# Optimization experiments

Hardware: AMD Instinct MI355X
Metric: run time of the kernel (lower is better)

The kernel has to match this reference:

```python
import jax, jax.numpy as jnp
import numpy as np

MESSAGE_PASSES = 3
HID = 100        # hidden_node_features == message_size
EDGE_F = 4       # n_edge_features
OUT = 100        # readout output dim


def setup_inputs() -> dict:
    key = jax.random.key(0)
    ks = jax.random.split(key, 8)
    B, N = 32, 128
    nodes = jax.random.normal(ks[0], (B, N, HID), dtype=jnp.float32)
    edges = jax.random.uniform(ks[1], (B, N, N, EDGE_F), dtype=jnp.float32)
    s = 1.0 / np.sqrt(HID)
    Wv = jax.random.normal(ks[2], (HID, HID), dtype=jnp.float32) * s
    Ww = jax.random.normal(ks[3], (HID, HID), dtype=jnp.float32) * s
    We = jax.random.normal(ks[4], (EDGE_F, HID), dtype=jnp.float32) * (1.0 / np.sqrt(EDGE_F))
    Wu = jax.random.normal(ks[5], (2 * HID, HID), dtype=jnp.float32) * (1.0 / np.sqrt(2 * HID))
    Wr = jax.random.normal(ks[6], (2 * HID, OUT), dtype=jnp.float32) * (1.0 / np.sqrt(2 * HID))
    return {"nodes": nodes, "edges": edges, "Wv": Wv, "Ww": Ww, "We": We, "Wu": Wu, "Wr": Wr}


def reference(nodes, edges, Wv, Ww, We, Wu, Wr):
    # adjacency[b,v,w] = sum_e edges[b,v,w,e]; nonzero entries define the edge set
    adjacency = edges.sum(axis=-1)                       # [B,N,N]
    edge_mask = adjacency != 0                           # [B,N,N]
    node_mask = adjacency.sum(axis=-1) != 0              # [B,N]

    # edge feature projection is constant across message passes
    e_proj = jnp.einsum('bvwe,eh->bvwh', edges, We)      # [B,N,N,H]

    hidden = nodes                                       # hidden_node_features == node feat dim
    for _ in range(MESSAGE_PASSES):
        # message_terms for every (b, v, w) edge: relu(h_v Wv + h_w Ww + e_vw We)
        pre = (hidden @ Wv)[:, :, None, :] + (hidden @ Ww)[:, None, :, :] + e_proj
        mterms = jnp.where(edge_mask[..., None], jax.nn.relu(pre), 0.0)
        # (same_batch * same_node) matmul == segment-sum over neighbors w
        messages = mterms.sum(axis=2)                    # [B,N,H]
        # update only nodes that appear in the edge set (degree > 0)
        upd = jnp.tanh(jnp.concatenate([hidden, messages], axis=-1) @ Wu)
        hidden = jnp.where(node_mask[..., None], upd, hidden)

    # readout: masked sum-pool of per-node graph terms
    graph_terms = jax.nn.relu(jnp.concatenate([hidden, nodes], axis=-1) @ Wr)  # [B,N,OUT]
    output = jnp.where(node_mask[..., None], graph_terms, 0.0).sum(axis=1)     # [B,OUT]
    return output
```

## Files before the change

### kernel.cpp

```cpp
#include <hip/hip_runtime.h>
#include <math.h>

#define BATCH 32
#define N 128
#define H 100
#define EF 4

__global__ __launch_bounds__(128) void k_hw(const float* __restrict__ hidden,
                                            const float* __restrict__ Ww,
                                            float* __restrict__ hw) {
    const int row = blockIdx.x;
    const int t = threadIdx.x;
    __shared__ float hid[H];
    if (t < H) hid[t] = hidden[row * H + t];
    __syncthreads();
    if (t < H) {
        float acc = 0.f;
#pragma unroll 4
        for (int k = 0; k < H; ++k) acc = fmaf(hid[k], Ww[k * H + t], acc);
        hw[row * H + t] = acc;
    }
}

__global__ __launch_bounds__(128) void k_msg_upd(const float* __restrict__ edges,
                                                 const float* __restrict__ Wv,
                                                 const float* __restrict__ We,
                                                 const float* __restrict__ Wu,
                                                 const float* __restrict__ hw,
                                                 float* __restrict__ hidden,
                                                 float* __restrict__ node_mask) {
    const int row = blockIdx.x;
    const int b = row >> 7;
    const int t = threadIdx.x;

    __shared__ float hid[H];
    __shared__ float4 erow[N];
    __shared__ float asum[N];
    __shared__ float msg[H];
    __shared__ float nodesum;

    if (t < H) hid[t] = hidden[row * H + t];
    {
        const float4* e4 = (const float4*)(edges + (size_t)row * N * EF);
        float4 e = e4[t];
        erow[t] = e;
        asum[t] = ((e.x + e.y) + e.z) + e.w;
    }
    __syncthreads();

    if (t == 0) {
        float s = 0.f;
        for (int w = 0; w < N; ++w) s += asum[w];
        nodesum = s;
        node_mask[row] = (s != 0.f) ? 1.f : 0.f;
    }

    if (t < H) {
        float hv = 0.f;
#pragma unroll 4
        for (int k = 0; k < H; ++k) hv = fmaf(hid[k], Wv[k * H + t], hv);

        const float we0 = We[t];
        const float we1 = We[H + t];
        const float we2 = We[2 * H + t];
        const float we3 = We[3 * H + t];

        const float* hwb = hw + (size_t)b * N * H + t;
        float acc = 0.f;
#pragma unroll 4
        for (int w = 0; w < N; ++w) {
            const float4 e = erow[w];
            float pre = hv + hwb[w * H];
            pre = fmaf(e.x, we0, pre);
            pre = fmaf(e.y, we1, pre);
            pre = fmaf(e.z, we2, pre);
            pre = fmaf(e.w, we3, pre);
            acc += (asum[w] != 0.f) ? fmaxf(pre, 0.f) : 0.f;
        }
        msg[t] = acc;
    }
    __syncthreads();

    if (t < H) {
        float u = 0.f;
#pragma unroll 4
        for (int k = 0; k < H; ++k) u = fmaf(hid[k], Wu[k * H + t], u);
#pragma unroll 4
        for (int k = 0; k < H; ++k) u = fmaf(msg[k], Wu[(H + k) * H + t], u);
        const float newh = (nodesum != 0.f) ? tanhf(u) : hid[t];
        hidden[row * H + t] = newh;
    }
}

__global__ __launch_bounds__(128) void k_readout(const float* __restrict__ hidden,
                                                 const float* __restrict__ nodes,
                                                 const float* __restrict__ Wr,
                                                 const float* __restrict__ node_mask,
                                                 float* __restrict__ out) {
    const int row = blockIdx.x;
    const int b = row >> 7;
    const int t = threadIdx.x;
    __shared__ float hid[H];
    __shared__ float nod[H];
    if (t < H) {
        hid[t] = hidden[row * H + t];
        nod[t] = nodes[row * H + t];
    }
    __syncthreads();
    if (node_mask[row] == 0.f) return;
    if (t < H) {
        float u = 0.f;
#pragma unroll 4
        for (int k = 0; k < H; ++k) u = fmaf(hid[k], Wr[k * H + t], u);
#pragma unroll 4
        for (int k = 0; k < H; ++k) u = fmaf(nod[k], Wr[(H + k) * H + t], u);
        u = fmaxf(u, 0.f);
        atomicAdd(&out[b * H + t], u);
    }
}

extern "C" void kernel_launch(void* const* d_in, const int* in_sizes, int n_in,
                              void* d_out, int out_size, void* d_ws, size_t ws_size,
                              hipStream_t stream) {
    const float* nodes = (const float*)d_in[0];
    const float* edges = (const float*)d_in[1];
    const float* Wv    = (const float*)d_in[2];
    const float* Ww    = (const float*)d_in[3];
    const float* We    = (const float*)d_in[4];
    const float* Wu    = (const float*)d_in[5];
    const float* Wr    = (const float*)d_in[6];
    float* out = (float*)d_out;

    const int rows = BATCH * N;
    float* hidden = (float*)d_ws;
    float* hwbuf  = hidden + (size_t)rows * H;
    float* nmask  = hwbuf + (size_t)rows * H;

    hipMemcpyAsync(hidden, nodes, (size_t)rows * H * sizeof(float),
                   hipMemcpyDeviceToDevice, stream);
    hipMemsetAsync(d_out, 0, (size_t)out_size * sizeof(float), stream);

    for (int p = 0; p < 3; ++p) {
        k_hw<<<rows, 128, 0, stream>>>(hidden, Ww, hwbuf);
        k_msg_upd<<<rows, 128, 0, stream>>>(edges, Wv, We, Wu, hwbuf, hidden, nmask);
    }
    k_readout<<<rows, 128, 0, stream>>>(hidden, nodes, Wr, nmask, out);
}
```

Before: 238.1 us.

## Tile eight nodes per block, stage neighbor projections in LDS, fuse next-pass projection

Each block now processes eight nodes of one graph, with two output columns per thread. Neighbor hW rows are staged in shared memory in two 64-row halves and reused across the eight nodes, instead of every node re-reading all of hW from global memory. The next pass's hv/hw projections are fused into the update kernel using ping-pong hw buffers, and the node mask moves to a separate wave-reduction kernel. Readout reduces over the eight nodes in shared memory before issuing atomics. The cost is more shared memory per block (about 34 KB), some idle threads (448 threads for 400 active), and more workspace buffers.

```diff
diff --git a/kernel.cpp b/kernel.cpp
--- a/kernel.cpp
+++ b/kernel.cpp
@@ -1,121 +1,228 @@
 #include <hip/hip_runtime.h>
 #include <math.h>
 
-#define BATCH 32
-#define N 128
-#define H 100
-#define EF 4
-
-__global__ __launch_bounds__(128) void k_hw(const float* __restrict__ hidden,
-                                            const float* __restrict__ Ww,
-                                            float* __restrict__ hw) {
-    const int row = blockIdx.x;
-    const int t = threadIdx.x;
-    __shared__ float hid[H];
-    if (t < H) hid[t] = hidden[row * H + t];
-    __syncthreads();
-    if (t < H) {
-        float acc = 0.f;
-#pragma unroll 4
-        for (int k = 0; k < H; ++k) acc = fmaf(hid[k], Ww[k * H + t], acc);
-        hw[row * H + t] = acc;
-    }
-}
-
-__global__ __launch_bounds__(128) void k_msg_upd(const float* __restrict__ edges,
-                                                 const float* __restrict__ Wv,
-                                                 const float* __restrict__ We,
-                                                 const float* __restrict__ Wu,
-                                                 const float* __restrict__ hw,
-                                                 float* __restrict__ hidden,
-                                                 float* __restrict__ node_mask) {
-    const int row = blockIdx.x;
-    const int b = row >> 7;
-    const int t = threadIdx.x;
-
-    __shared__ float hid[H];
-    __shared__ float4 erow[N];
-    __shared__ float asum[N];
-    __shared__ float msg[H];
-    __shared__ float nodesum;
-
-    if (t < H) hid[t] = hidden[row * H + t];
-    {
-        const float4* e4 = (const float4*)(edges + (size_t)row * N * EF);
-        float4 e = e4[t];
-        erow[t] = e;
-        asum[t] = ((e.x + e.y) + e.z) + e.w;
-    }
-    __syncthreads();
-
-    if (t == 0) {
-        float s = 0.f;
-        for (int w = 0; w < N; ++w) s += asum[w];
-        nodesum = s;
-        node_mask[row] = (s != 0.f) ? 1.f : 0.f;
-    }
-
-    if (t < H) {
-        float hv = 0.f;
-#pragma unroll 4
-        for (int k = 0; k < H; ++k) hv = fmaf(hid[k], Wv[k * H + t], hv);
-
-        const float we0 = We[t];
-        const float we1 = We[H + t];
-        const float we2 = We[2 * H + t];
-        const float we3 = We[3 * H + t];
-
-        const float* hwb = hw + (size_t)b * N * H + t;
-        float acc = 0.f;
-#pragma unroll 4
-        for (int w = 0; w < N; ++w) {
-            const float4 e = erow[w];
-            float pre = hv + hwb[w * H];
-            pre = fmaf(e.x, we0, pre);
-            pre = fmaf(e.y, we1, pre);
-            pre = fmaf(e.z, we2, pre);
-            pre = fmaf(e.w, we3, pre);
-            acc += (asum[w] != 0.f) ? fmaxf(pre, 0.f) : 0.f;
-        }
-        msg[t] = acc;
-    }
-    __syncthreads();
-
-    if (t < H) {
-        float u = 0.f;
-#pragma unroll 4
-        for (int k = 0; k < H; ++k) u = fmaf(hid[k], Wu[k * H + t], u);
-#pragma unroll 4
-        for (int k = 0; k < H; ++k) u = fmaf(msg[k], Wu[(H + k) * H + t], u);
-        const float newh = (nodesum != 0.f) ? tanhf(u) : hid[t];
-        hidden[row * H + t] = newh;
-    }
-}
-
-__global__ __launch_bounds__(128) void k_readout(const float* __restrict__ hidden,
+#define B_   32
+#define N_   128
+#define H_   100
+#define VT   8
+#define TPB  448
+#define ROWS (B_ * N_)
+
+__global__ __launch_bounds__(256) void k_mask(const float* __restrict__ edges,
+                                              float* __restrict__ nmask) {
+    const int t = threadIdx.x, lane = t & 63, wv = t >> 6;
+    const int row = blockIdx.x * 4 + wv;
+    const float4* eg = (const float4*)(edges + (size_t)row * N_ * 4);
+    float4 e0 = eg[lane], e1 = eg[lane + 64];
+    float s = ((e0.x + e0.y) + (e0.z + e0.w)) + ((e1.x + e1.y) + (e1.z + e1.w));
+#pragma unroll
+    for (int off = 32; off > 0; off >>= 1) s += __shfl_down(s, off);
+    if (lane == 0) nmask[row] = (s != 0.f) ? 1.f : 0.f;
+}
+
+__global__ __launch_bounds__(TPB) void k_proj0(const float* __restrict__ nodes,
+                                               const float* __restrict__ Wv,
+                                               const float* __restrict__ Ww,
+                                               float* __restrict__ hv_out,
+                                               float* __restrict__ hw_out) {
+    __shared__ float hid_s[VT * H_];
+    const int b = blockIdx.y, v0 = blockIdx.x * VT;
+    const int t = threadIdx.x, v = t / 50, hp = t % 50;
+    const bool act = (v < VT);
+    const int row = b * N_ + v0 + (act ? v : 0);
+
+    const float4* ng = (const float4*)(nodes + (size_t)(b * N_ + v0) * H_);
+    for (int idx = t; idx < VT * 25; idx += TPB) ((float4*)hid_s)[idx] = ng[idx];
+    __syncthreads();
+    if (!act) return;
+
+    const float2* Wv2 = (const float2*)Wv;
+    const float2* Ww2 = (const float2*)Ww;
+    float va0 = 0, va1 = 0, wa0 = 0, wa1 = 0;
+    const float* hr = hid_s + v * H_;
+#pragma unroll 4
+    for (int k = 0; k < H_; ++k) {
+        const float hk = hr[k];
+        const float2 wv = Wv2[k * 50 + hp];
+        const float2 ww = Ww2[k * 50 + hp];
+        va0 = fmaf(hk, wv.x, va0); va1 = fmaf(hk, wv.y, va1);
+        wa0 = fmaf(hk, ww.x, wa0); wa1 = fmaf(hk, ww.y, wa1);
+    }
+    *(float2*)(hv_out + (size_t)row * H_ + hp * 2) = make_float2(va0, va1);
+    *(float2*)(hw_out + (size_t)row * H_ + hp * 2) = make_float2(wa0, wa1);
+}
+
+__global__ __launch_bounds__(TPB) void k_pass(const float* __restrict__ edges,
+                                              const float* __restrict__ Wv,
+                                              const float* __restrict__ Ww,
+                                              const float* __restrict__ We,
+                                              const float* __restrict__ Wu,
+                                              const float* hv_io,
+                                              const float* __restrict__ hw_in,
+                                              float* __restrict__ hw_out,
+                                              float* __restrict__ hidden,
+                                              const float* __restrict__ nmask,
+                                              int do_proj) {
+    __shared__ float  hw_s[64 * H_];
+    __shared__ float4 e_s[VT * 64];
+    __shared__ float  mask_s[VT * 64];
+    __shared__ float  hid_s[VT * H_];
+
+    const int b = blockIdx.y, v0 = blockIdx.x * VT;
+    const int t = threadIdx.x, v = t / 50, hp = t % 50;
+    const bool act = (v < VT);
+    const int row = b * N_ + v0 + (act ? v : 0);
+
+    float2 hv2 = make_float2(0.f, 0.f), we0, we1, we2, we3;
+    if (act) {
+        hv2 = *(const float2*)(hv_io + (size_t)row * H_ + hp * 2);
+        we0 = *(const float2*)(We + 0 * H_ + hp * 2);
+        we1 = *(const float2*)(We + 1 * H_ + hp * 2);
+        we2 = *(const float2*)(We + 2 * H_ + hp * 2);
+        we3 = *(const float2*)(We + 3 * H_ + hp * 2);
+    }
+    float a0 = 0.f, a1 = 0.f;
+
+    for (int half = 0; half < 2; ++half) {
+        const int w0 = half * 64;
+        __syncthreads();
+        {
+            const float4* hwg = (const float4*)(hw_in + (size_t)(b * N_ + w0) * H_);
+            float4* hws4 = (float4*)hw_s;
+            for (int idx = t; idx < 64 * 25; idx += TPB) hws4[idx] = hwg[idx];
+        }
+        {
+            const float4* eg = (const float4*)edges;
+            for (int idx = t; idx < VT * 64; idx += TPB) {
+                const int vv = idx >> 6, w = idx & 63;
+                const float4 e = eg[(size_t)(b * N_ + v0 + vv) * N_ + w0 + w];
+                e_s[vv * 64 + w] = e;
+                const float s = ((e.x + e.y) + (e.z + e.w));
+                mask_s[vv * 64 + w] = (s != 0.f) ? 1.f : 0.f;
+            }
+        }
+        if (half == 0) {
+            const float4* hg = (const float4*)(hidden + (size_t)(b * N_ + v0) * H_);
+            for (int idx = t; idx < VT * 25; idx += TPB) ((float4*)hid_s)[idx] = hg[idx];
+        }
+        __syncthreads();
+        if (act) {
+            const float4* ev = e_s + v * 64;
+            const float*  mv = mask_s + v * 64;
+#pragma unroll 4
+            for (int w = 0; w < 64; ++w) {
+                const float4 e = ev[w];
+                const float  m = mv[w];
+                const float2 hw2 = *(const float2*)(hw_s + w * H_ + hp * 2);
+                float p0 = hv2.x + hw2.x, p1 = hv2.y + hw2.y;
+                p0 = fmaf(e.x, we0.x, p0); p1 = fmaf(e.x, we0.y, p1);
+                p0 = fmaf(e.y, we1.x, p0); p1 = fmaf(e.y, we1.y, p1);
+                p0 = fmaf(e.z, we2.x, p0); p1 = fmaf(e.z, we2.y, p1);
+                p0 = fmaf(e.w, we3.x, p0); p1 = fmaf(e.w, we3.y, p1);
+                a0 = fmaf(m, fmaxf(p0, 0.f), a0);
+                a1 = fmaf(m, fmaxf(p1, 0.f), a1);
+            }
+        }
+    }
+
+    __syncthreads();
+    float* msg_s = (float*)e_s;
+    if (act) *(float2*)(msg_s + v * H_ + hp * 2) = make_float2(a0, a1);
+    __syncthreads();
+
+    float2 nh = make_float2(0.f, 0.f);
+    if (act) {
+        const float2* Wu2 = (const float2*)Wu;
+        float u0 = 0.f, u1 = 0.f;
+        const float* hr = hid_s + v * H_;
+        const float* mr = msg_s + v * H_;
+#pragma unroll 4
+        for (int k = 0; k < H_; ++k) {
+            const float hk = hr[k];
+            const float2 wu = Wu2[k * 50 + hp];
+            u0 = fmaf(hk, wu.x, u0); u1 = fmaf(hk, wu.y, u1);
+        }
+#pragma unroll 4
+        for (int k = 0; k < H_; ++k) {
+            const float mk = mr[k];
+            const float2 wu = Wu2[(H_ + k) * 50 + hp];
+            u0 = fmaf(mk, wu.x, u0); u1 = fmaf(mk, wu.y, u1);
+        }
+        const float nm = nmask[row];
+        const float h0 = hr[hp * 2], h1 = hr[hp * 2 + 1];
+        nh.x = (nm != 0.f) ? tanhf(u0) : h0;
+        nh.y = (nm != 0.f) ? tanhf(u1) : h1;
+        *(float2*)(hidden + (size_t)row * H_ + hp * 2) = nh;
+    }
+
+    if (do_proj) {
+        float* hn_s = hw_s;
+        __syncthreads();
+        if (act) *(float2*)(hn_s + v * H_ + hp * 2) = nh;
+        __syncthreads();
+        if (act) {
+            const float2* Wv2 = (const float2*)Wv;
+            const float2* Ww2 = (const float2*)Ww;
+            float va0 = 0, va1 = 0, wa0 = 0, wa1 = 0;
+            const float* hr = hn_s + v * H_;
+#pragma unroll 4
+            for (int k = 0; k < H_; ++k) {
+                const float hk = hr[k];
+                const float2 wv = Wv2[k * 50 + hp];
+                const float2 ww = Ww2[k * 50 + hp];
+                va0 = fmaf(hk, wv.x, va0); va1 = fmaf(hk, wv.y, va1);
+                wa0 = fmaf(hk, ww.x, wa0); wa1 = fmaf(hk, ww.y, wa1);
+            }
+            *(float2*)((float*)hv_io + (size_t)row * H_ + hp * 2) = make_float2(va0, va1);
+            *(float2*)(hw_out + (size_t)row * H_ + hp * 2) = make_float2(wa0, wa1);
+        }
+    }
+}
+
+__global__ __launch_bounds__(TPB) void k_readout(const float* __restrict__ hidden,
                                                  const float* __restrict__ nodes,
                                                  const float* __restrict__ Wr,
-                                                 const float* __restrict__ node_mask,
+                                                 const float* __restrict__ nmask,
                                                  float* __restrict__ out) {
-    const int row = blockIdx.x;
-    const int b = row >> 7;
-    const int t = threadIdx.x;
-    __shared__ float hid[H];
-    __shared__ float nod[H];
-    if (t < H) {
-        hid[t] = hidden[row * H + t];
-        nod[t] = nodes[row * H + t];
-    }
-    __syncthreads();
-    if (node_mask[row] == 0.f) return;
-    if (t < H) {
-        float u = 0.f;
-#pragma unroll 4
-        for (int k = 0; k < H; ++k) u = fmaf(hid[k], Wr[k * H + t], u);
-#pragma unroll 4
-        for (int k = 0; k < H; ++k) u = fmaf(nod[k], Wr[(H + k) * H + t], u);
-        u = fmaxf(u, 0.f);
-        atomicAdd(&out[b * H + t], u);
+    __shared__ float hid_s[VT * H_], nod_s[VT * H_], red_s[VT * H_];
+    const int b = blockIdx.y, v0 = blockIdx.x * VT;
+    const int t = threadIdx.x, v = t / 50, hp = t % 50;
+    const bool act = (v < VT);
+    const int row = b * N_ + v0 + (act ? v : 0);
+
+    const float4* hg = (const float4*)(hidden + (size_t)(b * N_ + v0) * H_);
+    const float4* ng = (const float4*)(nodes + (size_t)(b * N_ + v0) * H_);
+    for (int idx = t; idx < VT * 25; idx += TPB) ((float4*)hid_s)[idx] = hg[idx];
+    for (int idx = t; idx < VT * 25; idx += TPB) ((float4*)nod_s)[idx] = ng[idx];
+    __syncthreads();
+
+    if (act) {
+        const float2* Wr2 = (const float2*)Wr;
+        float u0 = 0.f, u1 = 0.f;
+        const float* hr = hid_s + v * H_;
+        const float* nr = nod_s + v * H_;
+#pragma unroll 4
+        for (int k = 0; k < H_; ++k) {
+            const float hk = hr[k];
+            const float2 wr = Wr2[k * 50 + hp];
+            u0 = fmaf(hk, wr.x, u0); u1 = fmaf(hk, wr.y, u1);
+        }
+#pragma unroll 4
+        for (int k = 0; k < H_; ++k) {
+            const float nk = nr[k];
+            const float2 wr = Wr2[(H_ + k) * 50 + hp];
+            u0 = fmaf(nk, wr.x, u0); u1 = fmaf(nk, wr.y, u1);
+        }
+        const float m = nmask[row];
+        red_s[v * H_ + hp * 2]     = m * fmaxf(u0, 0.f);
+        red_s[v * H_ + hp * 2 + 1] = m * fmaxf(u1, 0.f);
+    }
+    __syncthreads();
+    if (t < H_) {
+        float s = 0.f;
+#pragma unroll
+        for (int vv = 0; vv < VT; ++vv) s += red_s[vv * H_ + t];
+        atomicAdd(out + b * H_ + t, s);
     }
 }
 
@@ -131,18 +238,21 @@
     const float* Wr    = (const float*)d_in[6];
     float* out = (float*)d_out;
 
-    const int rows = BATCH * N;
+    const size_t RH = (size_t)ROWS * H_;
     float* hidden = (float*)d_ws;
-    float* hwbuf  = hidden + (size_t)rows * H;
-    float* nmask  = hwbuf + (size_t)rows * H;
-
-    hipMemcpyAsync(hidden, nodes, (size_t)rows * H * sizeof(float),
-                   hipMemcpyDeviceToDevice, stream);
+    float* hv     = hidden + RH;
+    float* hwA    = hv + RH;
+    float* hwB    = hwA + RH;
+    float* nmask  = hwB + RH;
+
+    hipMemcpyAsync(hidden, nodes, RH * sizeof(float), hipMemcpyDeviceToDevice, stream);
     hipMemsetAsync(d_out, 0, (size_t)out_size * sizeof(float), stream);
 
-    for (int p = 0; p < 3; ++p) {
-        k_hw<<<rows, 128, 0, stream>>>(hidden, Ww, hwbuf);
-        k_msg_upd<<<rows, 128, 0, stream>>>(edges, Wv, We, Wu, hwbuf, hidden, nmask);
-    }
-    k_readout<<<rows, 128, 0, stream>>>(hidden, nodes, Wr, nmask, out);
-}
+    const dim3 grid(N_ / VT, B_);
+    k_mask<<<ROWS / 4, 256, 0, stream>>>(edges, nmask);
+    k_proj0<<<grid, TPB, 0, stream>>>(nodes, Wv, Ww, hv, hwA);
+    k_pass<<<grid, TPB, 0, stream>>>(edges, Wv, Ww, We, Wu, hv, hwA, hwB, hidden, nmask, 1);
+    k_pass<<<grid, TPB, 0, stream>>>(edges, Wv, Ww, We, Wu, hv, hwB, hwA, hidden, nmask, 1);
+    k_pass<<<grid, TPB, 0, stream>>>(edges, Wv, Ww, We, Wu, hv, hwA, hwB, hidden, nmask, 0);
+    k_readout<<<grid, TPB, 0, stream>>>(hidden, nodes, Wr, nmask, out);
+}
```

Result: slower. 263.6 us (+10.7%).
